# Performance work log

Hardware: AMD Instinct MI355X
Metric: run time of the kernel (lower is better)

Reference implementation:

```python
import jax, jax.numpy as jnp
import numpy as np

DIM = 64
KSIZE = 3
BN_EPS = 1e-5

def _bn(x):
    # eval-mode BatchNorm2d with default running stats (mean=0, var=1) and affine (1, 0)
    return x / jnp.sqrt(1.0 + BN_EPS)

def _downsample(x, params):
    # four stride-2 3x3 convs: 3 -> 8 -> 16 -> 32 -> 64, BN after each, GELU except after last
    for i, (w, b) in enumerate(params):
        x = jax.lax.conv_general_dilated(x, w, (2, 2), ((1, 1), (1, 1))) + b[None, :, None, None]
        x = _bn(x)
        if i < 3:
            x = jax.nn.gelu(x, approximate=False)
    return x

def _attn(dx, q, kw, kb, vw, vb, pw, pb, dw, db):
    # single-head cross attention: learned queries q (1,T,C) attend to dx (B,N,C)
    scale = DIM ** -0.5
    k = dx @ kw.T + kb
    v = dx @ vw.T + vb
    a = jax.nn.softmax((q @ jnp.swapaxes(k, -1, -2)) * scale, axis=-1)  # (B,T,N)
    o = (a @ v) @ pw.T + pb                                            # (B,T,C)
    return o @ dw.T + db                                               # (B,T,1)

def _gk1d(sigma):
    half = (KSIZE - 1) * 0.5
    x = jnp.linspace(-half, half, KSIZE)
    pdf = jnp.exp(-0.5 * (x / sigma) ** 2)
    return pdf / pdf.sum()

def _gain_denoise(I1, r1, r2, gain, sigma):
    # per-image gain + gaussian-blur unsharp masking, vectorized over the batch
    def one(img, r1i, r2i, gi, si):
        ig = gi * img                                       # (3,H,W)
        k2 = _gk1d(r2i)[:, None] * _gk1d(r1i)[None, :]      # (k,k), sigma_x=r1, sigma_y=r2
        kern = jnp.broadcast_to(k2, (3, 1, KSIZE, KSIZE))   # depthwise kernel
        p = KSIZE // 2
        xp = jnp.pad(ig[None], ((0, 0), (0, 0), (p, p), (p, p)), mode='reflect')
        blur = jax.lax.conv_general_dilated(xp, kern, (1, 1), 'VALID', feature_group_count=3)[0]
        return blur + si * (img - blur)
    return jax.vmap(one)(I1, r1, r2, gain, sigma)

def setup_inputs():
    key = jax.random.key(0)
    ks = iter(jax.random.split(key, 64))
    def rn(shape, s=0.05):
        return jax.random.normal(next(ks), shape, dtype=jnp.float32) * s
    def ru(shape):
        return jax.random.uniform(next(ks), shape, dtype=jnp.float32)
    inp = {"I1": ru((8, 3, 512, 512))}
    for pre, T in (("kp", 4), ("mp", 10)):
        inp[pre + "_q"] = ru((1, T, DIM))
        chans = [3, DIM // 8, DIM // 4, DIM // 2, DIM]
        for i in range(4):
            inp[pre + "_c%dw" % (i + 1)] = rn((chans[i + 1], chans[i], 3, 3), 0.1)
            inp[pre + "_c%db" % (i + 1)] = jnp.zeros((chans[i + 1],), jnp.float32)
        for nm, shp in (("kw", (DIM, DIM)), ("vw", (DIM, DIM)), ("pw", (DIM, DIM)), ("dw", (1, DIM))):
            inp[pre + "_" + nm] = rn(shp)
        for nm, n in (("kb", DIM), ("vb", DIM), ("pb", DIM), ("db", 1)):
            inp[pre + "_" + nm] = jnp.zeros((n,), jnp.float32)
    inp["kp_gain_base"] = jnp.ones((1,), jnp.float32)  # mode='normal'
    dims = [3, 32, 32, 32, 32, 3]
    for i in range(5):
        inp["lut_w%d" % i] = rn((dims[i + 1], dims[i]), 0.2)
        inp["lut_b%d" % i] = jnp.zeros((dims[i + 1],), jnp.float32)
    return inp

def reference(I1, kp_q, kp_c1w, kp_c1b, kp_c2w, kp_c2b, kp_c3w, kp_c3b, kp_c4w, kp_c4b,
              kp_kw, kp_kb, kp_vw, kp_vb, kp_pw, kp_pb, kp_dw, kp_db, kp_gain_base,
              mp_q, mp_c1w, mp_c1b, mp_c2w, mp_c2b, mp_c3w, mp_c3b, mp_c4w, mp_c4b,
              mp_kw, mp_kb, mp_vw, mp_vb, mp_pw, mp_pb, mp_dw, mp_db,
              lut_w0, lut_b0, lut_w1, lut_b1, lut_w2, lut_b2, lut_w3, lut_b3, lut_w4, lut_b4):
    B = I1.shape[0]
    # --- Kernel_Predictor ---
    dx = _downsample(I1, [(kp_c1w, kp_c1b), (kp_c2w, kp_c2b), (kp_c3w, kp_c3b), (kp_c4w, kp_c4b)])
    dx = dx.reshape(B, DIM, -1).transpose(0, 2, 1)            # (B,N,C), N=(H/16)*(W/16)
    o = _attn(dx, kp_q, kp_kw, kp_kb, kp_vw, kp_vb, kp_pw, kp_pb, kp_dw, kp_db)[..., 0]  # (B,4)
    r1 = 0.1 * o[:, 0] + 3.0
    r2 = 0.1 * o[:, 1] + 2.0
    gain = o[:, 2] + kp_gain_base[0]
    sigma = jax.nn.sigmoid(o[:, 3])
    # --- gain + gaussian unsharp denoise ---
    I2 = jnp.clip(_gain_denoise(I1, r1, r2, gain, sigma), 1e-5, 1.0)
    # --- Matrix_Predictor ---
    dx2 = _downsample(I2, [(mp_c1w, mp_c1b), (mp_c2w, mp_c2b), (mp_c3w, mp_c3b), (mp_c4w, mp_c4b)])
    dx2 = dx2.reshape(B, DIM, -1).transpose(0, 2, 1)
    o2 = _attn(dx2, mp_q, mp_kw, mp_kb, mp_vw, mp_vb, mp_pw, mp_pb, mp_dw, mp_db)  # (B,10,1)
    ccm = 0.1 * o2[:, :9, 0].reshape(B, 3, 3) + jnp.eye(3, dtype=I1.dtype)
    dist = jax.nn.relu(o2[:, 9, 0]) + 1.0                     # (B,)
    # --- Shades-of-Gray white balance + CCM ---
    hwc = I2.transpose(0, 2, 3, 1)                            # (B,H,W,3)
    imgP = hwc ** dist[:, None, None, None]
    ch = jnp.mean(imgP, axis=(1, 2)) ** (1.0 / dist)[:, None]  # (B,3)
    avg = jnp.mean(imgP, axis=(1, 2, 3)) ** (1.0 / dist)       # (B,)
    I3 = hwc / (ch / avg[:, None])[:, None, None, :]
    I4 = jnp.clip(jnp.einsum('bhwc,bdc->bhwd', I3, ccm), 1e-5, 1.0)
    # --- NILUT residual per-pixel MLP ---
    h = jax.nn.relu(I4 @ lut_w0.T + lut_b0)
    h = jnp.tanh(h @ lut_w1.T + lut_b1)
    h = jnp.tanh(h @ lut_w2.T + lut_b2)
    h = jnp.tanh(h @ lut_w3.T + lut_b3)
    I5 = jnp.clip(h @ lut_w4.T + lut_b4 + I4, 0.0, 1.0)
    return I5.transpose(0, 3, 1, 2)                           # (B,3,H,W)
```

## Files before the change

kernel.cpp:

```cpp
#include <hip/hip_runtime.h>
#include <math.h>


#define BN_MUL 0.9999950000374997f

static constexpr int BB   = 8;
static constexpr int HH   = 512;
static constexpr int WW   = 512;
static constexpr int HW   = HH * WW;
static constexpr int NTOK = 1024;
static constexpr int DIMC = 64;
static constexpr int WBCH = 32;
static constexpr int LUTN = 33;
static constexpr int LUTT = LUTN * LUTN * LUTN;

__device__ __forceinline__ float gelu_exact(float x) {
    return 0.5f * x * (1.0f + erff(x * 0.7071067811865476f));
}

__device__ __forceinline__ float tanh_fast(float x) {
    float e = __expf(2.0f * x);
    return 1.0f - 2.0f * __builtin_amdgcn_rcpf(e + 1.0f);
}

template<int Cin, int Hin, int OCT, bool GELU>
__global__ __launch_bounds__(256) void conv_s2(const float* __restrict__ in,
                                               const float* __restrict__ wt,
                                               const float* __restrict__ bs,
                                               float* __restrict__ out)
{
    constexpr int Win  = Hin, Hout = Hin / 2, Wout = Hin / 2;
    constexpr int WSH  = (Wout == 256) ? 8 : (Wout == 128) ? 7 : (Wout == 64) ? 6 : 5;
    constexpr int PLANE = Hout * Wout;

    const int sp  = blockIdx.x * 256 + threadIdx.x;
    const int ow  = sp & (Wout - 1);
    const int oh  = sp >> WSH;
    const int oc0 = blockIdx.y * OCT;
    const int b   = blockIdx.z;
    const int Cout = (int)gridDim.y * OCT;

    float acc[OCT];
    #pragma unroll
    for (int o = 0; o < OCT; ++o) acc[o] = bs[oc0 + o];

    const int ih0 = oh * 2 - 1, iw0 = ow * 2 - 1;
    const float fh0 = (ih0 >= 0) ? 1.f : 0.f;
    const float fw0 = (iw0 >= 0) ? 1.f : 0.f;
    const int r0 = (ih0 >= 0) ? ih0 : 0;
    const int cc0 = (iw0 >= 0) ? iw0 : 0;

    const float* ip = in + (size_t)(b * Cin) * Hin * Win;
    #pragma unroll
    for (int ic = 0; ic < Cin; ++ic) {
        const float* pl = ip + ic * Hin * Win;
        const float* p0 = pl + r0 * Win;
        const float* p1 = pl + (ih0 + 1) * Win;
        const float* p2 = pl + (ih0 + 2) * Win;
        float  v00 = p0[cc0] * (fh0 * fw0);
        float2 va  = *(const float2*)(p0 + iw0 + 1);
        float  v01 = va.x * fh0, v02 = va.y * fh0;
        float  v10 = p1[cc0] * fw0;
        float2 vb  = *(const float2*)(p1 + iw0 + 1);
        float  v20 = p2[cc0] * fw0;
        float2 vc  = *(const float2*)(p2 + iw0 + 1);
        #pragma unroll
        for (int o = 0; o < OCT; ++o) {
            const float* wr = wt + ((oc0 + o) * Cin + ic) * 9;
            acc[o] += v00 * wr[0] + v01 * wr[1] + v02 * wr[2]
                    + v10 * wr[3] + vb.x * wr[4] + vb.y * wr[5]
                    + v20 * wr[6] + vc.x * wr[7] + vc.y * wr[8];
        }
    }
    #pragma unroll
    for (int o = 0; o < OCT; ++o) {
        float a = acc[o] * BN_MUL;
        if (GELU) a = gelu_exact(a);
        out[(size_t)(b * Cout + oc0 + o) * PLANE + sp] = a;
    }
}

__global__ __launch_bounds__(256) void denoise_conv1_kernel(
    const float* __restrict__ I1, const float* __restrict__ attno,
    const float* __restrict__ gain_base,
    const float* __restrict__ wt, const float* __restrict__ bs,
    float* __restrict__ I2, float* __restrict__ out)
{
    const int sp = blockIdx.x * 256 + threadIdx.x;
    const int ow = sp & 255;
    const int oh = sp >> 8;
    const int b  = blockIdx.z;

    const float o0 = attno[b * 4 + 0], o1 = attno[b * 4 + 1];
    const float o2 = attno[b * 4 + 2], o3 = attno[b * 4 + 3];
    const float r1 = 0.1f * o0 + 3.0f;
    const float r2 = 0.1f * o1 + 2.0f;
    const float g  = o2 + gain_base[0];
    const float sg = 1.0f / (1.0f + __expf(-o3));
    const float ex = __expf(-0.5f / (r1 * r1));
    const float nx = 1.0f / (2.0f * ex + 1.0f);
    const float ey = __expf(-0.5f / (r2 * r2));
    const float ny = 1.0f / (2.0f * ey + 1.0f);
    const float kx0 = ex * nx, kx1 = nx;
    const float ky0 = ey * ny, ky1 = ny;

    const int rbase = 2 * oh - 2, cbase = 2 * ow - 2;
    int ri[5], ci[5];
    #pragma unroll
    for (int i = 0; i < 5; ++i) {
        int r = rbase + i; ri[i] = r < 0 ? -r : (r > 511 ? 1022 - r : r);
        int c = cbase + i; ci[i] = c < 0 ? -c : (c > 511 ? 1022 - c : c);
    }
    const bool topE = (oh == 0), leftE = (ow == 0);

    float acc[8];
    #pragma unroll
    for (int o = 0; o < 8; ++o) acc[o] = bs[o];

    #pragma unroll
    for (int c = 0; c < 3; ++c) {
        const float* ip = I1 + ((size_t)b * 3 + c) * HW;
        float p[5][5];
        #pragma unroll
        for (int i = 0; i < 5; ++i) {
            const float* rp = ip + ri[i] * WW;
            #pragma unroll
            for (int j = 0; j < 5; ++j) p[i][j] = rp[ci[j]];
        }
        float hs[5][3];
        #pragma unroll
        for (int i = 0; i < 5; ++i)
            #pragma unroll
            for (int j = 0; j < 3; ++j)
                hs[i][j] = kx0 * (p[i][j] + p[i][j + 2]) + kx1 * p[i][j + 1];
        float w2[3][3];
        #pragma unroll
        for (int i = 0; i < 3; ++i)
            #pragma unroll
            for (int j = 0; j < 3; ++j) {
                float bl = g * (ky0 * (hs[i][j] + hs[i + 2][j]) + ky1 * hs[i + 1][j]);
                float val = bl + sg * (p[i + 1][j + 1] - bl);
                w2[i][j] = fminf(fmaxf(val, 1e-5f), 1.0f);
            }
        float* op = I2 + ((size_t)b * 3 + c) * HW + (2 * oh) * WW + 2 * ow;
        float2 w0v; w0v.x = w2[1][1]; w0v.y = w2[1][2];
        float2 w1v; w1v.x = w2[2][1]; w1v.y = w2[2][2];
        *(float2*)op        = w0v;
        *(float2*)(op + WW) = w1v;
        if (topE)  { w2[0][0] = 0.f; w2[0][1] = 0.f; w2[0][2] = 0.f; }
        if (leftE) { w2[0][0] = 0.f; w2[1][0] = 0.f; w2[2][0] = 0.f; }
        #pragma unroll
        for (int o = 0; o < 8; ++o) {
            const float* wr = wt + (o * 3 + c) * 9;
            acc[o] += w2[0][0] * wr[0] + w2[0][1] * wr[1] + w2[0][2] * wr[2]
                    + w2[1][0] * wr[3] + w2[1][1] * wr[4] + w2[1][2] * wr[5]
                    + w2[2][0] * wr[6] + w2[2][1] * wr[7] + w2[2][2] * wr[8];
        }
    }
    #pragma unroll
    for (int o = 0; o < 8; ++o)
        out[(b * 8 + o) * 65536 + sp] = gelu_exact(acc[o] * BN_MUL);
}

__global__ __launch_bounds__(1024) void attn_kernel(
    const float* __restrict__ dx, const float* __restrict__ q,
    const float* __restrict__ kw, const float* __restrict__ kb,
    const float* __restrict__ vw, const float* __restrict__ vb,
    const float* __restrict__ pw, const float* __restrict__ pb,
    const float* __restrict__ dw, const float* __restrict__ db,
    float* __restrict__ outv, int T)
{
    __shared__ float qk[DIMC];
    __shared__ float sc[NTOK];
    __shared__ float wredm[16];
    __shared__ float wreds[16];
    __shared__ float uN[DIMC];
    __shared__ float osh[DIMC];
    __shared__ float psh[DIMC];
    __shared__ float qkb_s;
    const int tid  = threadIdx.x;
    const int lane = tid & 63;
    const int wv   = tid >> 6;
    const int bt   = blockIdx.x;
    const int b = bt / T, t = bt - b * T;
    const float* qt = q + t * DIMC;

    if (tid < DIMC) {
        float s = 0.f;
        #pragma unroll
        for (int c = 0; c < DIMC; ++c) s += qt[c] * kw[c * DIMC + tid];
        qk[tid] = s;
    }
    if (tid == 1023) {
        float s = 0.f;
        #pragma unroll
        for (int c = 0; c < DIMC; ++c) s += qt[c] * kb[c];
        qkb_s = s;
    }
    __syncthreads();

    const float* dp = dx + (size_t)(b * DIMC) * NTOK;
    float s = qkb_s;
    #pragma unroll
    for (int c = 0; c < DIMC; ++c) s += qk[c] * dp[c * NTOK + tid];
    s *= 0.125f;

    float m = s;
    #pragma unroll
    for (int off = 32; off > 0; off >>= 1) m = fmaxf(m, __shfl_xor(m, off));
    if (lane == 0) wredm[wv] = m;
    __syncthreads();
    m = wredm[0];
    #pragma unroll
    for (int k = 1; k < 16; ++k) m = fmaxf(m, wredm[k]);

    float e = __expf(s - m);
    sc[tid] = e;
    float ss = e;
    #pragma unroll
    for (int off = 32; off > 0; off >>= 1) ss += __shfl_xor(ss, off);
    if (lane == 0) wreds[wv] = ss;
    __syncthreads();
    float Ssum = wreds[0];
    #pragma unroll
    for (int k = 1; k < 16; ++k) Ssum += wreds[k];

    #pragma unroll
    for (int cc = 0; cc < 4; ++cc) {
        const int c = wv * 4 + cc;
        const float* dr = dp + c * NTOK;
        float p = 0.f;
        #pragma unroll
        for (int k = 0; k < 16; ++k) p += sc[k * 64 + lane] * dr[k * 64 + lane];
        #pragma unroll
        for (int off = 32; off > 0; off >>= 1) p += __shfl_xor(p, off);
        if (lane == 0) uN[c] = p / Ssum;
    }
    __syncthreads();

    if (tid < DIMC) {
        float o = vb[tid];
        const float* vr = vw + tid * DIMC;
        #pragma unroll
        for (int cc = 0; cc < DIMC; ++cc) o += vr[cc] * uN[cc];
        osh[tid] = o;
    }
    __syncthreads();
    if (tid < DIMC) {
        float p = pb[tid];
        const float* pr = pw + tid * DIMC;
        #pragma unroll
        for (int cc = 0; cc < DIMC; ++cc) p += pr[cc] * osh[cc];
        psh[tid] = p;
    }
    __syncthreads();
    if (tid == 0) {
        float r = db[0];
        #pragma unroll
        for (int cc = 0; cc < DIMC; ++cc) r += psh[cc] * dw[cc];
        outv[bt] = r;
    }
}

__global__ __launch_bounds__(256) void nilut_build_kernel(
    const float* __restrict__ w0, const float* __restrict__ b0,
    const float* __restrict__ w1, const float* __restrict__ b1,
    const float* __restrict__ w2, const float* __restrict__ b2,
    const float* __restrict__ w3, const float* __restrict__ b3,
    const float* __restrict__ w4, const float* __restrict__ b4,
    float4* __restrict__ table)
{
    __shared__ __align__(16) float sw[3][1024];
    __shared__ float sw0[96], sw4[96];
    __shared__ float sb[4][32];
    __shared__ float sb4[3];
    const int t = threadIdx.x;

    for (int i = t; i < 1024; i += 256) {
        sw[0][i] = w1[i];
        sw[1][i] = w2[i];
        sw[2][i] = w3[i];
    }
    if (t < 96) { sw0[t] = w0[t]; sw4[t] = w4[t]; }
    if (t < 32) { sb[0][t] = b0[t]; sb[1][t] = b1[t]; sb[2][t] = b2[t]; sb[3][t] = b3[t]; }
    if (t == 255) { sb4[0] = b4[0]; sb4[1] = b4[1]; sb4[2] = b4[2]; }
    __syncthreads();

    const int idx = blockIdx.x * 256 + t;
    if (idx >= LUTT) return;
    const int c0 = idx % LUTN;
    const int c1 = (idx / LUTN) % LUTN;
    const int c2 = idx / (LUTN * LUTN);
    const float v0 = (float)c0 * (1.0f / 32.0f);
    const float v1 = (float)c1 * (1.0f / 32.0f);
    const float v2 = (float)c2 * (1.0f / 32.0f);

    float h[32], g[32];
    #pragma unroll
    for (int j = 0; j < 32; ++j)
        h[j] = fmaxf(sb[0][j] + sw0[j*3] * v0 + sw0[j*3+1] * v1 + sw0[j*3+2] * v2, 0.f);

    #pragma unroll
    for (int L = 0; L < 3; ++L) {
        #pragma unroll
        for (int j = 0; j < 32; ++j) {
            float a = sb[L + 1][j];
            const float4* wr = (const float4*)&sw[L][j * 32];
            #pragma unroll
            for (int k4 = 0; k4 < 8; ++k4) {
                float4 w = wr[k4];
                a += w.x * h[k4*4] + w.y * h[k4*4+1] + w.z * h[k4*4+2] + w.w * h[k4*4+3];
            }
            g[j] = tanh_fast(a);
        }
        #pragma unroll
        for (int j = 0; j < 32; ++j) h[j] = g[j];
    }

    float4 r;
    float o[3];
    #pragma unroll
    for (int d = 0; d < 3; ++d) {
        float a = sb4[d];
        #pragma unroll
        for (int k = 0; k < 32; ++k) a += sw4[d * 32 + k] * h[k];
        o[d] = a;
    }
    r.x = o[0]; r.y = o[1]; r.z = o[2]; r.w = 0.f;
    table[idx] = r;
}

__global__ __launch_bounds__(256) void wb_reduce_kernel(
    const float* __restrict__ I2, const float* __restrict__ attno,
    float* __restrict__ part, unsigned* __restrict__ cnt,
    float* __restrict__ wbsc)
{
    __shared__ float red[256];
    __shared__ int lastf;
    const int bc = blockIdx.y;
    const int b  = bc / 3;
    float d = attno[b * 10 + 9];
    d = fmaxf(d, 0.f) + 1.0f;
    constexpr int CHUNK = HW / WBCH;
    const float4* base = (const float4*)(I2 + (size_t)bc * HW + blockIdx.x * CHUNK);
    float l = 0.f;
    #pragma unroll
    for (int i = threadIdx.x, it = 0; it < CHUNK / 4 / 256; ++it, i += 256) {
        float4 v = base[i];
        l += __expf(d * __logf(v.x)) + __expf(d * __logf(v.y))
           + __expf(d * __logf(v.z)) + __expf(d * __logf(v.w));
    }
    red[threadIdx.x] = l;
    __syncthreads();
    for (int off = 128; off > 0; off >>= 1) {
        if (threadIdx.x < off) red[threadIdx.x] += red[threadIdx.x + off];
        __syncthreads();
    }
    if (threadIdx.x == 0) {
        part[bc * WBCH + blockIdx.x] = red[0];
        __threadfence();
        unsigned g = atomicAdd(cnt, 1u);
        lastf = ((g % 768u) == 767u) ? 1 : 0;
    }
    __syncthreads();
    if (!lastf) return;
    __threadfence();

    const int t = threadIdx.x;
    if (t < BB) {
        const int bb = t;
        float dd = attno[bb * 10 + 9];
        dd = fmaxf(dd, 0.f) + 1.0f;
        float inv = 1.0f / dd;
        float s[3];
        #pragma unroll
        for (int c = 0; c < 3; ++c) {
            float t0 = 0.f;
            const float* pp = part + (bb * 3 + c) * WBCH;
            #pragma unroll
            for (int k = 0; k < WBCH; ++k) t0 += pp[k];
            s[c] = t0;
        }
        float avg = powf((s[0] + s[1] + s[2]) / (3.0f * (float)HW), inv);
        #pragma unroll
        for (int c = 0; c < 3; ++c)
            wbsc[bb * 4 + c] = avg / powf(s[c] / (float)HW, inv);
    }
}

__global__ void __launch_bounds__(256) final_kernel(
    float* __restrict__ io,
    const float* __restrict__ wbsc, const float* __restrict__ attno,
    const float4* __restrict__ table)
{
    const int tid = threadIdx.x;
    const int b   = blockIdx.x >> 10;
    const int pix = (blockIdx.x * 256 + tid) & (HW - 1);
    float* base = io + b * 3 * HW + pix;

    const float s0 = wbsc[b * 4 + 0], s1 = wbsc[b * 4 + 1], s2 = wbsc[b * 4 + 2];
    float v0 = base[0] * s0;
    float v1 = base[HW] * s1;
    float v2 = base[2 * HW] * s2;
    const float* o2p = attno + b * 10;
    float I4[3];
    #pragma unroll
    for (int d = 0; d < 3; ++d) {
        float m0 = 0.1f * o2p[d * 3]     + (d == 0 ? 1.f : 0.f);
        float m1 = 0.1f * o2p[d * 3 + 1] + (d == 1 ? 1.f : 0.f);
        float m2 = 0.1f * o2p[d * 3 + 2] + (d == 2 ? 1.f : 0.f);
        I4[d] = fminf(fmaxf(m0 * v0 + m1 * v1 + m2 * v2, 1e-5f), 1.0f);
    }

    float p0 = I4[0] * 32.0f, p1 = I4[1] * 32.0f, p2 = I4[2] * 32.0f;
    int i0 = (int)p0; i0 = i0 > 31 ? 31 : i0;
    int i1 = (int)p1; i1 = i1 > 31 ? 31 : i1;
    int i2 = (int)p2; i2 = i2 > 31 ? 31 : i2;
    float f0 = p0 - (float)i0, f1 = p1 - (float)i1, f2 = p2 - (float)i2;

    const int ib = (i2 * LUTN + i1) * LUTN + i0;
    float4 c000 = table[ib],              c100 = table[ib + 1];
    float4 c010 = table[ib + LUTN],       c110 = table[ib + LUTN + 1];
    float4 c001 = table[ib + LUTN*LUTN],  c101 = table[ib + LUTN*LUTN + 1];
    float4 c011 = table[ib + LUTN*LUTN + LUTN];
    float4 c111 = table[ib + LUTN*LUTN + LUTN + 1];

    float r[3];
    {
        float x00 = c000.x + f0 * (c100.x - c000.x);
        float x10 = c010.x + f0 * (c110.x - c010.x);
        float x01 = c001.x + f0 * (c101.x - c001.x);
        float x11 = c011.x + f0 * (c111.x - c011.x);
        float y0 = x00 + f1 * (x10 - x00);
        float y1 = x01 + f1 * (x11 - x01);
        r[0] = y0 + f2 * (y1 - y0);
    }
    {
        float x00 = c000.y + f0 * (c100.y - c000.y);
        float x10 = c010.y + f0 * (c110.y - c010.y);
        float x01 = c001.y + f0 * (c101.y - c001.y);
        float x11 = c011.y + f0 * (c111.y - c011.y);
        float y0 = x00 + f1 * (x10 - x00);
        float y1 = x01 + f1 * (x11 - x01);
        r[1] = y0 + f2 * (y1 - y0);
    }
    {
        float x00 = c000.z + f0 * (c100.z - c000.z);
        float x10 = c010.z + f0 * (c110.z - c010.z);
        float x01 = c001.z + f0 * (c101.z - c001.z);
        float x11 = c011.z + f0 * (c111.z - c011.z);
        float y0 = x00 + f1 * (x10 - x00);
        float y1 = x01 + f1 * (x11 - x01);
        r[2] = y0 + f2 * (y1 - y0);
    }

    #pragma unroll
    for (int d = 0; d < 3; ++d)
        base[d * HW] = fminf(fmaxf(I4[d] + r[d], 0.f), 1.0f);
}

extern "C" void kernel_launch(void* const* d_in, const int* in_sizes, int n_in,
                              void* d_out, int out_size, void* d_ws, size_t ws_size,
                              hipStream_t stream)
{
    const float* I1      = (const float*)d_in[0];
    const float* kp_q    = (const float*)d_in[1];
    const float* kp_c1w  = (const float*)d_in[2];  const float* kp_c1b = (const float*)d_in[3];
    const float* kp_c2w  = (const float*)d_in[4];  const float* kp_c2b = (const float*)d_in[5];
    const float* kp_c3w  = (const float*)d_in[6];  const float* kp_c3b = (const float*)d_in[7];
    const float* kp_c4w  = (const float*)d_in[8];  const float* kp_c4b = (const float*)d_in[9];
    const float* kp_kw   = (const float*)d_in[10]; const float* kp_vw  = (const float*)d_in[11];
    const float* kp_pw   = (const float*)d_in[12]; const float* kp_dw  = (const float*)d_in[13];
    const float* kp_kb   = (const float*)d_in[14]; const float* kp_vb  = (const float*)d_in[15];
    const float* kp_pb   = (const float*)d_in[16]; const float* kp_db  = (const float*)d_in[17];
    const float* mp_q    = (const float*)d_in[18];
    const float* mp_c1w  = (const float*)d_in[19]; const float* mp_c1b = (const float*)d_in[20];
    const float* mp_c2w  = (const float*)d_in[21]; const float* mp_c2b = (const float*)d_in[22];
    const float* mp_c3w  = (const float*)d_in[23]; const float* mp_c3b = (const float*)d_in[24];
    const float* mp_c4w  = (const float*)d_in[25]; const float* mp_c4b = (const float*)d_in[26];
    const float* mp_kw   = (const float*)d_in[27]; const float* mp_vw  = (const float*)d_in[28];
    const float* mp_pw   = (const float*)d_in[29]; const float* mp_dw  = (const float*)d_in[30];
    const float* mp_kb   = (const float*)d_in[31]; const float* mp_vb  = (const float*)d_in[32];
    const float* mp_pb   = (const float*)d_in[33]; const float* mp_db  = (const float*)d_in[34];
    const float* gainb   = (const float*)d_in[35];
    const float* lw0 = (const float*)d_in[36]; const float* lb0 = (const float*)d_in[37];
    const float* lw1 = (const float*)d_in[38]; const float* lb1 = (const float*)d_in[39];
    const float* lw2 = (const float*)d_in[40]; const float* lb2 = (const float*)d_in[41];
    const float* lw3 = (const float*)d_in[42]; const float* lb3 = (const float*)d_in[43];
    const float* lw4 = (const float*)d_in[44]; const float* lb4 = (const float*)d_in[45];

    float* ws    = (float*)d_ws;
    float* ds1   = ws;
    float* ds2   = ds1 + 8 * 8 * 256 * 256;
    float* ds3   = ds2 + 8 * 16 * 128 * 128;
    float* ds4   = ds3 + 8 * 32 * 64 * 64;
    float* attno = ds4 + 8 * 64 * 32 * 32;
    float* part  = attno + 128;
    float* wbsc  = part + 24 * WBCH;
    unsigned* wbcnt = (unsigned*)(wbsc + 32);
    float* I2    = (float*)d_out;
    float4* table = (float4*)ds1;

    conv_s2<3, 512, 8, true ><<<dim3(256, 1, BB), 256, 0, stream>>>(I1,  kp_c1w, kp_c1b, ds1);
    conv_s2<8, 256, 8, true ><<<dim3(64,  2, BB), 256, 0, stream>>>(ds1, kp_c2w, kp_c2b, ds2);
    conv_s2<16, 128, 4, true><<<dim3(16,  8, BB), 256, 0, stream>>>(ds2, kp_c3w, kp_c3b, ds3);
    conv_s2<32, 64, 4, false><<<dim3(4,  16, BB), 256, 0, stream>>>(ds3, kp_c4w, kp_c4b, ds4);
    attn_kernel<<<BB * 4, 1024, 0, stream>>>(ds4, kp_q, kp_kw, kp_kb, kp_vw, kp_vb,
                                             kp_pw, kp_pb, kp_dw, kp_db, attno, 4);

    denoise_conv1_kernel<<<dim3(256, 1, BB), 256, 0, stream>>>(I1, attno, gainb,
                                                               mp_c1w, mp_c1b, I2, ds1);

    conv_s2<8, 256, 8, true ><<<dim3(64,  2, BB), 256, 0, stream>>>(ds1, mp_c2w, mp_c2b, ds2);
    nilut_build_kernel<<<(LUTT + 255) / 256, 256, 0, stream>>>(
        lw0, lb0, lw1, lb1, lw2, lb2, lw3, lb3, lw4, lb4, table);
    conv_s2<16, 128, 4, true><<<dim3(16,  8, BB), 256, 0, stream>>>(ds2, mp_c3w, mp_c3b, ds3);
    conv_s2<32, 64, 4, false><<<dim3(4,  32 / 2, BB), 256, 0, stream>>>(ds3, mp_c4w, mp_c4b, ds4);
    attn_kernel<<<BB * 10, 1024, 0, stream>>>(ds4, mp_q, mp_kw, mp_kb, mp_vw, mp_vb,
                                              mp_pw, mp_pb, mp_dw, mp_db, attno, 10);

    wb_reduce_kernel<<<dim3(WBCH, 24), 256, 0, stream>>>(I2, attno, part, wbcnt, wbsc);

    final_kernel<<<BB * HW / 256, 256, 0, stream>>>(I2, wbsc, attno, table);
}
```

Baseline: 409.1 us.

## Fuse conv layers 2-4 into one tiled kernel and merge LUT build into it

Replaces the separate stride-2 conv2, conv3 and conv4 launches with a single kernel. Each block computes a tile of the 32x32 output and keeps the intermediate conv2/conv3 halos in shared memory, so ds2/ds3 no longer round-trip through global memory and two launches per branch are removed. The NILUT table build is folded into the same grid as extra blocks so it runs alongside the predictor convs, and the table is moved to ds2, which is now free. The cost is redundant halo recomputation of conv2 and conv3 plus a larger shared-memory footprint per block, which may reduce occupancy.

```diff
diff --git a/kernel.cpp b/kernel.cpp
--- a/kernel.cpp
+++ b/kernel.cpp
@@ -77,6 +77,194 @@
         float a = acc[o] * BN_MUL;
         if (GELU) a = gelu_exact(a);
         out[(size_t)(b * Cout + oc0 + o) * PLANE + sp] = a;
+    }
+}
+
+__global__ __launch_bounds__(256) void conv234_kernel(
+    const float* __restrict__ in,
+    const float* __restrict__ w2, const float* __restrict__ b2,
+    const float* __restrict__ w3, const float* __restrict__ b3,
+    const float* __restrict__ w4, const float* __restrict__ b4,
+    float* __restrict__ out,
+    const float* __restrict__ lw0, const float* __restrict__ lb0,
+    const float* __restrict__ lw1, const float* __restrict__ lb1,
+    const float* __restrict__ lw2, const float* __restrict__ lb2,
+    const float* __restrict__ lw3, const float* __restrict__ lb3,
+    const float* __restrict__ lw4, const float* __restrict__ lb4,
+    float4* __restrict__ table)
+{
+    __shared__ float s2[16][209];
+    __shared__ float s3[32][45];
+    __shared__ __align__(16) float sw[3][1024];
+    __shared__ float sw0[96], sw4[96];
+    __shared__ float sb[4][32];
+    __shared__ float sb4[3];
+
+    const int t   = threadIdx.x;
+    const int bid = blockIdx.x;
+
+    if (bid >= 1024) {
+        for (int i = t; i < 1024; i += 256) {
+            sw[0][i] = lw1[i];
+            sw[1][i] = lw2[i];
+            sw[2][i] = lw3[i];
+        }
+        if (t < 96) { sw0[t] = lw0[t]; sw4[t] = lw4[t]; }
+        if (t < 32) { sb[0][t] = lb0[t]; sb[1][t] = lb1[t]; sb[2][t] = lb2[t]; sb[3][t] = lb3[t]; }
+        if (t == 255) { sb4[0] = lb4[0]; sb4[1] = lb4[1]; sb4[2] = lb4[2]; }
+        __syncthreads();
+
+        const int idx = (bid - 1024) * 256 + t;
+        if (idx >= LUTT) return;
+        const int c0 = idx % LUTN;
+        const int c1 = (idx / LUTN) % LUTN;
+        const int c2 = idx / (LUTN * LUTN);
+        const float v0 = (float)c0 * (1.0f / 32.0f);
+        const float v1 = (float)c1 * (1.0f / 32.0f);
+        const float v2 = (float)c2 * (1.0f / 32.0f);
+
+        float h[32], g[32];
+        #pragma unroll
+        for (int j = 0; j < 32; ++j)
+            h[j] = fmaxf(sb[0][j] + sw0[j*3] * v0 + sw0[j*3+1] * v1 + sw0[j*3+2] * v2, 0.f);
+        #pragma unroll
+        for (int L = 0; L < 3; ++L) {
+            #pragma unroll
+            for (int j = 0; j < 32; ++j) {
+                float a = sb[L + 1][j];
+                const float4* wr = (const float4*)&sw[L][j * 32];
+                #pragma unroll
+                for (int k4 = 0; k4 < 8; ++k4) {
+                    float4 w = wr[k4];
+                    a += w.x * h[k4*4] + w.y * h[k4*4+1] + w.z * h[k4*4+2] + w.w * h[k4*4+3];
+                }
+                g[j] = tanh_fast(a);
+            }
+            #pragma unroll
+            for (int j = 0; j < 32; ++j) h[j] = g[j];
+        }
+        float4 r;
+        float o[3];
+        #pragma unroll
+        for (int d = 0; d < 3; ++d) {
+            float a = sb4[d];
+            #pragma unroll
+            for (int k = 0; k < 32; ++k) a += sw4[d * 32 + k] * h[k];
+            o[d] = a;
+        }
+        r.x = o[0]; r.y = o[1]; r.z = o[2]; r.w = 0.f;
+        table[idx] = r;
+        return;
+    }
+
+    const int b  = bid >> 7;
+    const int bx = bid & 127;
+    const int tx = bx & 7, ty = bx >> 3;
+
+    for (int unit = t; unit < 418; unit += 256) {
+        const int px = (unit < 209) ? unit : unit - 209;
+        const int cg = (unit < 209) ? 0 : 1;
+        const int y2l = px / 19, x2l = px - y2l * 19;
+        const int y2 = 8 * ty - 3 + y2l;
+        const int x2 = 16 * tx - 3 + x2l;
+        if ((unsigned)y2 < 128u && (unsigned)x2 < 128u) {
+            float acc[8];
+            #pragma unroll
+            for (int o = 0; o < 8; ++o) acc[o] = b2[cg * 8 + o];
+            const int ih0 = 2 * y2 - 1, iw0 = 2 * x2 - 1;
+            const float fh0 = (ih0 >= 0) ? 1.f : 0.f;
+            const float fw0 = (iw0 >= 0) ? 1.f : 0.f;
+            const int r0  = (ih0 >= 0) ? ih0 : 0;
+            const int cc0 = (iw0 >= 0) ? iw0 : 0;
+            const float* ip = in + (size_t)(b * 8) * 65536;
+            #pragma unroll
+            for (int ic = 0; ic < 8; ++ic) {
+                const float* pl = ip + ic * 65536;
+                const float* p0 = pl + r0 * 256;
+                const float* p1 = pl + (ih0 + 1) * 256;
+                const float* p2 = pl + (ih0 + 2) * 256;
+                float  v00 = p0[cc0] * (fh0 * fw0);
+                float2 va  = *(const float2*)(p0 + iw0 + 1);
+                float  v01 = va.x * fh0, v02 = va.y * fh0;
+                float  v10 = p1[cc0] * fw0;
+                float2 vb  = *(const float2*)(p1 + iw0 + 1);
+                float  v20 = p2[cc0] * fw0;
+                float2 vc  = *(const float2*)(p2 + iw0 + 1);
+                #pragma unroll
+                for (int o = 0; o < 8; ++o) {
+                    const float* wr = w2 + ((cg * 8 + o) * 8 + ic) * 9;
+                    acc[o] += v00 * wr[0] + v01 * wr[1] + v02 * wr[2]
+                            + v10 * wr[3] + vb.x * wr[4] + vb.y * wr[5]
+                            + v20 * wr[6] + vc.x * wr[7] + vc.y * wr[8];
+                }
+            }
+            #pragma unroll
+            for (int o = 0; o < 8; ++o)
+                s2[cg * 8 + o][px] = gelu_exact(acc[o] * BN_MUL);
+        } else {
+            #pragma unroll
+            for (int o = 0; o < 8; ++o) s2[cg * 8 + o][px] = 0.f;
+        }
+    }
+    __syncthreads();
+
+    if (t < 180) {
+        const int px = t % 45, cg = t / 45;
+        const int y3l = px / 9, x3l = px - y3l * 9;
+        const int y3 = 4 * ty - 1 + y3l;
+        const int x3 = 8 * tx - 1 + x3l;
+        if ((unsigned)y3 < 64u && (unsigned)x3 < 64u) {
+            float acc[8];
+            #pragma unroll
+            for (int j = 0; j < 8; ++j) acc[j] = b3[cg * 8 + j];
+            #pragma unroll
+            for (int ic = 0; ic < 16; ++ic) {
+                const float* sp = &s2[ic][(2 * y3l) * 19 + 2 * x3l];
+                float v0 = sp[0],  v1 = sp[1],  v2 = sp[2];
+                float v3 = sp[19], v4 = sp[20], v5 = sp[21];
+                float v6 = sp[38], v7 = sp[39], v8 = sp[40];
+                #pragma unroll
+                for (int j = 0; j < 8; ++j) {
+                    const float* wr = w3 + ((cg * 8 + j) * 16 + ic) * 9;
+                    acc[j] += v0 * wr[0] + v1 * wr[1] + v2 * wr[2]
+                            + v3 * wr[3] + v4 * wr[4] + v5 * wr[5]
+                            + v6 * wr[6] + v7 * wr[7] + v8 * wr[8];
+                }
+            }
+            #pragma unroll
+            for (int j = 0; j < 8; ++j)
+                s3[cg * 8 + j][px] = gelu_exact(acc[j] * BN_MUL);
+        } else {
+            #pragma unroll
+            for (int j = 0; j < 8; ++j) s3[cg * 8 + j][px] = 0.f;
+        }
+    }
+    __syncthreads();
+
+    {
+        const int px = t & 7, cg = t >> 3;
+        const int y4l = px >> 2, x4l = px & 3;
+        const int y4 = 2 * ty + y4l, x4 = 4 * tx + x4l;
+        const int oc0 = cg * 2;
+        float a0 = b4[oc0], a1 = b4[oc0 + 1];
+        #pragma unroll
+        for (int ic = 0; ic < 32; ++ic) {
+            const float* sp = &s3[ic][(2 * y4l) * 9 + 2 * x4l];
+            float v0 = sp[0],  v1 = sp[1],  v2 = sp[2];
+            float v3 = sp[9],  v4 = sp[10], v5 = sp[11];
+            float v6 = sp[18], v7 = sp[19], v8 = sp[20];
+            const float* wr0 = w4 + (oc0 * 32 + ic) * 9;
+            const float* wr1 = w4 + ((oc0 + 1) * 32 + ic) * 9;
+            a0 += v0 * wr0[0] + v1 * wr0[1] + v2 * wr0[2]
+                + v3 * wr0[3] + v4 * wr0[4] + v5 * wr0[5]
+                + v6 * wr0[6] + v7 * wr0[7] + v8 * wr0[8];
+            a1 += v0 * wr1[0] + v1 * wr1[1] + v2 * wr1[2]
+                + v3 * wr1[3] + v4 * wr1[4] + v5 * wr1[5]
+                + v6 * wr1[6] + v7 * wr1[7] + v8 * wr1[8];
+        }
+        float* op = out + (size_t)(b * 64 + oc0) * 1024 + y4 * 32 + x4;
+        op[0]    = a0 * BN_MUL;
+        op[1024] = a1 * BN_MUL;
     }
 }
 
@@ -260,74 +448,6 @@
         for (int cc = 0; cc < DIMC; ++cc) r += psh[cc] * dw[cc];
         outv[bt] = r;
     }
-}
-
-__global__ __launch_bounds__(256) void nilut_build_kernel(
-    const float* __restrict__ w0, const float* __restrict__ b0,
-    const float* __restrict__ w1, const float* __restrict__ b1,
-    const float* __restrict__ w2, const float* __restrict__ b2,
-    const float* __restrict__ w3, const float* __restrict__ b3,
-    const float* __restrict__ w4, const float* __restrict__ b4,
-    float4* __restrict__ table)
-{
-    __shared__ __align__(16) float sw[3][1024];
-    __shared__ float sw0[96], sw4[96];
-    __shared__ float sb[4][32];
-    __shared__ float sb4[3];
-    const int t = threadIdx.x;
-
-    for (int i = t; i < 1024; i += 256) {
-        sw[0][i] = w1[i];
-        sw[1][i] = w2[i];
-        sw[2][i] = w3[i];
-    }
-    if (t < 96) { sw0[t] = w0[t]; sw4[t] = w4[t]; }
-    if (t < 32) { sb[0][t] = b0[t]; sb[1][t] = b1[t]; sb[2][t] = b2[t]; sb[3][t] = b3[t]; }
-    if (t == 255) { sb4[0] = b4[0]; sb4[1] = b4[1]; sb4[2] = b4[2]; }
-    __syncthreads();
-
-    const int idx = blockIdx.x * 256 + t;
-    if (idx >= LUTT) return;
-    const int c0 = idx % LUTN;
-    const int c1 = (idx / LUTN) % LUTN;
-    const int c2 = idx / (LUTN * LUTN);
-    const float v0 = (float)c0 * (1.0f / 32.0f);
-    const float v1 = (float)c1 * (1.0f / 32.0f);
-    const float v2 = (float)c2 * (1.0f / 32.0f);
-
-    float h[32], g[32];
-    #pragma unroll
-    for (int j = 0; j < 32; ++j)
-        h[j] = fmaxf(sb[0][j] + sw0[j*3] * v0 + sw0[j*3+1] * v1 + sw0[j*3+2] * v2, 0.f);
-
-    #pragma unroll
-    for (int L = 0; L < 3; ++L) {
-        #pragma unroll
-        for (int j = 0; j < 32; ++j) {
-            float a = sb[L + 1][j];
-            const float4* wr = (const float4*)&sw[L][j * 32];
-            #pragma unroll
-            for (int k4 = 0; k4 < 8; ++k4) {
-                float4 w = wr[k4];
-                a += w.x * h[k4*4] + w.y * h[k4*4+1] + w.z * h[k4*4+2] + w.w * h[k4*4+3];
-            }
-            g[j] = tanh_fast(a);
-        }
-        #pragma unroll
-        for (int j = 0; j < 32; ++j) h[j] = g[j];
-    }
-
-    float4 r;
-    float o[3];
-    #pragma unroll
-    for (int d = 0; d < 3; ++d) {
-        float a = sb4[d];
-        #pragma unroll
-        for (int k = 0; k < 32; ++k) a += sw4[d * 32 + k] * h[k];
-        o[d] = a;
-    }
-    r.x = o[0]; r.y = o[1]; r.z = o[2]; r.w = 0.f;
-    table[idx] = r;
 }
 
 __global__ __launch_bounds__(256) void wb_reduce_kernel(
@@ -499,23 +619,24 @@
     float* wbsc  = part + 24 * WBCH;
     unsigned* wbcnt = (unsigned*)(wbsc + 32);
     float* I2    = (float*)d_out;
-    float4* table = (float4*)ds1;
-
-    conv_s2<3, 512, 8, true ><<<dim3(256, 1, BB), 256, 0, stream>>>(I1,  kp_c1w, kp_c1b, ds1);
-    conv_s2<8, 256, 8, true ><<<dim3(64,  2, BB), 256, 0, stream>>>(ds1, kp_c2w, kp_c2b, ds2);
-    conv_s2<16, 128, 4, true><<<dim3(16,  8, BB), 256, 0, stream>>>(ds2, kp_c3w, kp_c3b, ds3);
-    conv_s2<32, 64, 4, false><<<dim3(4,  16, BB), 256, 0, stream>>>(ds3, kp_c4w, kp_c4b, ds4);
+    float4* table = (float4*)ds2;
+
+    constexpr int BUILD_BLOCKS = (LUTT + 255) / 256;
+
+    conv_s2<3, 512, 8, true><<<dim3(256, 1, BB), 256, 0, stream>>>(I1, kp_c1w, kp_c1b, ds1);
+    conv234_kernel<<<1024, 256, 0, stream>>>(ds1,
+        kp_c2w, kp_c2b, kp_c3w, kp_c3b, kp_c4w, kp_c4b, ds4,
+        nullptr, nullptr, nullptr, nullptr, nullptr, nullptr,
+        nullptr, nullptr, nullptr, nullptr, nullptr);
     attn_kernel<<<BB * 4, 1024, 0, stream>>>(ds4, kp_q, kp_kw, kp_kb, kp_vw, kp_vb,
                                              kp_pw, kp_pb, kp_dw, kp_db, attno, 4);
 
     denoise_conv1_kernel<<<dim3(256, 1, BB), 256, 0, stream>>>(I1, attno, gainb,
                                                                mp_c1w, mp_c1b, I2, ds1);
 
-    conv_s2<8, 256, 8, true ><<<dim3(64,  2, BB), 256, 0, stream>>>(ds1, mp_c2w, mp_c2b, ds2);
-    nilut_build_kernel<<<(LUTT + 255) / 256, 256, 0, stream>>>(
+    conv234_kernel<<<1024 + BUILD_BLOCKS, 256, 0, stream>>>(ds1,
+        mp_c2w, mp_c2b, mp_c3w, mp_c3b, mp_c4w, mp_c4b, ds4,
         lw0, lb0, lw1, lb1, lw2, lb2, lw3, lb3, lw4, lb4, table);
-    conv_s2<16, 128, 4, true><<<dim3(16,  8, BB), 256, 0, stream>>>(ds2, mp_c3w, mp_c3b, ds3);
-    conv_s2<32, 64, 4, false><<<dim3(4,  32 / 2, BB), 256, 0, stream>>>(ds3, mp_c4w, mp_c4b, ds4);
     attn_kernel<<<BB * 10, 1024, 0, stream>>>(ds4, mp_q, mp_kw, mp_kb, mp_vw, mp_vb,
                                               mp_pw, mp_pb, mp_dw, mp_db, attno, 10);
 
```

New measurement: 1.191 ms. 2.91x slower.
